# Kernel optimization log

Hardware: AMD Instinct MI355X
Metric: run time of the kernel (lower is better)

The kernel has to match this reference:

```python
import jax, jax.numpy as jnp
import numpy as np

B, T, C = 4, 2048, 1024
H = 16
D = C // H  # head_dim = 64


def setup_inputs() -> dict:
    key = jax.random.key(0)
    k1, k2, k3, k4, k5 = jax.random.split(key, 5)
    s = 1.0 / np.sqrt(C)
    return {
        "x": jax.random.normal(k1, (B, T, C), dtype=jnp.float32),
        "Wqkv": jax.random.normal(k2, (C, 3 * C), dtype=jnp.float32) * s,
        "bqkv": jax.random.normal(k3, (3 * C,), dtype=jnp.float32) * 0.02,
        "Wproj": jax.random.normal(k4, (C, C), dtype=jnp.float32) * s,
        "bproj": jax.random.normal(k5, (C,), dtype=jnp.float32) * 0.02,
    }


def reference(x, Wqkv, bqkv, Wproj, bproj):
    b, t, c = x.shape
    qkv = x @ Wqkv + bqkv                      # [B,T,3C]
    qkv = qkv.reshape(b, t, 3, H, D)
    q, k, v = (qkv[:, :, i].transpose(0, 2, 1, 3) for i in range(3))  # [B,H,T,D]
    scale = D ** -0.5
    attn = jnp.einsum("bhqd,bhkd->bhqk", q, k) * scale
    causal = jnp.tril(jnp.ones((t, t), dtype=bool))
    attn = jnp.where(causal[None, None], attn, -jnp.inf)
    attn = jax.nn.softmax(attn, axis=-1)
    out = jnp.einsum("bhqk,bhkd->bhqd", attn, v)  # [B,H,T,D]
    out = out.transpose(0, 2, 1, 3).reshape(b, t, c)
    return out @ Wproj + bproj
```

## Files before the change

kernel.cpp:

```cpp
#include <hip/hip_runtime.h>
#include <hip/hip_bf16.h>

typedef __bf16 bf16;
typedef __bf16 bf16x4 __attribute__((ext_vector_type(4)));
typedef __bf16 bf16x8 __attribute__((ext_vector_type(8)));
typedef float  f32x4  __attribute__((ext_vector_type(4)));

#define DEV static __device__ __forceinline__

static constexpr int Bsz = 4, T = 2048, C = 1024, H = 16;
static constexpr int M  = Bsz * T;
static constexpr int N1 = 3 * C;
static constexpr float SM_SCALE = 0.125f;

DEV void gload16(const bf16* g, bf16* l) {
  __builtin_amdgcn_global_load_lds(
      (const __attribute__((address_space(1))) void*)g,
      (__attribute__((address_space(3))) void*)l, 16, 0, 0);
}

__launch_bounds__(256)
__global__ void convert_kernel(const float* __restrict__ in, bf16* __restrict__ out) {
  const size_t i = ((size_t)blockIdx.x * 256 + threadIdx.x) * 8;
  f32x4 a = *(const f32x4*)(in + i);
  f32x4 b = *(const f32x4*)(in + i + 4);
  *(bf16x4*)(out + i)     = __builtin_convertvector(a, bf16x4);
  *(bf16x4*)(out + i + 4) = __builtin_convertvector(b, bf16x4);
}

__launch_bounds__(256)
__global__ void transpose_conv_kernel(const float* __restrict__ in,
                                      bf16* __restrict__ out, int K, int N) {
  __shared__ float t[32][33];
  const int n0 = blockIdx.x * 32, k0 = blockIdx.y * 32;
  const int tx = threadIdx.x & 31, ty = threadIdx.x >> 5;
#pragma unroll
  for (int j = 0; j < 4; ++j)
    t[ty + j * 8][tx] = in[(size_t)(k0 + ty + j * 8) * N + n0 + tx];
  __syncthreads();
#pragma unroll
  for (int j = 0; j < 4; ++j)
    out[(size_t)(n0 + ty + j * 8) * K + k0 + tx] = (bf16)t[tx][ty + j * 8];
}

template <bool OUT_BF16>
__launch_bounds__(256)
__global__ void gemm_kernel(const bf16* __restrict__ A,
                            const bf16* __restrict__ Bt,
                            const float* __restrict__ bias,
                            void* __restrict__ Out, int Ndim, int Kdim) {
  __shared__ bf16 lds_a[128 * 64];
  __shared__ bf16 lds_b[128 * 64];
  const int tid = threadIdx.x;
  const int l = tid & 63, wid = tid >> 6;
  const int wm = wid >> 1, wn = wid & 1;
  const int lr = l & 15, lh = l >> 4;
  const int m0 = blockIdx.x * 128, n0 = blockIdx.y * 128;
  const int r8 = l >> 3, g8 = (l & 7) * 8;

  f32x4 acc[4][4] = {};

  for (int k0 = 0; k0 < Kdim; k0 += 64) {
    __syncthreads();
#pragma unroll
    for (int i = 0; i < 4; ++i) {
      const int c = wid * 4 + i;
      const int row = c * 8 + r8;
      gload16(A  + (size_t)(m0 + row) * Kdim + k0 + g8, &lds_a[c * 512]);
      gload16(Bt + (size_t)(n0 + row) * Kdim + k0 + g8, &lds_b[c * 512]);
    }
    __syncthreads();
#pragma unroll
    for (int kk = 0; kk < 2; ++kk) {
      bf16x8 af[4], bfr[4];
#pragma unroll
      for (int mi = 0; mi < 4; ++mi)
        af[mi] = *(const bf16x8*)&lds_a[(wm * 64 + mi * 16 + lr) * 64 + kk * 32 + lh * 8];
#pragma unroll
      for (int ni = 0; ni < 4; ++ni)
        bfr[ni] = *(const bf16x8*)&lds_b[(wn * 64 + ni * 16 + lr) * 64 + kk * 32 + lh * 8];
#pragma unroll
      for (int mi = 0; mi < 4; ++mi)
#pragma unroll
        for (int ni = 0; ni < 4; ++ni)
          acc[mi][ni] = __builtin_amdgcn_mfma_f32_16x16x32_bf16(
              af[mi], bfr[ni], acc[mi][ni], 0, 0, 0);
    }
  }
#pragma unroll
  for (int ni = 0; ni < 4; ++ni) {
    int col = n0 + wn * 64 + ni * 16 + lr;
    float bv = bias[col];
#pragma unroll
    for (int mi = 0; mi < 4; ++mi) {
#pragma unroll
      for (int r = 0; r < 4; ++r) {
        int row = m0 + wm * 64 + mi * 16 + lh * 4 + r;
        float v = acc[mi][ni][r] + bv;
        if (OUT_BF16)
          ((bf16*)Out)[(size_t)row * Ndim + col] = (bf16)v;
        else
          ((float*)Out)[(size_t)row * Ndim + col] = v;
      }
    }
  }
}

DEV int vswz(int d, int key) {
  return (d * 64 + key) ^ ((((d & 7) ^ (d >> 3)) & 7) << 3);
}

__launch_bounds__(256)
__global__ void attn_kernel(const bf16* __restrict__ qkv, bf16* __restrict__ out) {
  __shared__ bf16 lds_k[2][64 * 64];
  __shared__ bf16 lds_vt[2][64 * 64];
  __shared__ bf16 lds_p[4][16 * 64];
  const int tid = threadIdx.x, l = tid & 63, w = tid >> 6;
  const int lr = l & 15, lh = l >> 4;
  const int p = blockIdx.x;
  const int bh = p >> 4, jj = p & 15;
  const int b = bh >> 4, h = bh & 15;
  const size_t RS = 3 * C;
  const bf16* base  = qkv + (size_t)b * T * RS;
  const bf16* kbase = base + C + h * 64;
  const bf16* vbase = base + 2 * C + h * 64;
  const int srow = tid >> 3;
  const int ss   = tid & 7;
  bf16* op = out + (size_t)b * T * C + h * 64;

  for (int it = 0; it < 2; ++it) {
    const int qt = it ? jj : 31 - jj;
    const int q16 = qt * 64 + w * 16;
    bf16x8 qf[2];
#pragma unroll
    for (int kk = 0; kk < 2; ++kk) {
      bf16x8 qv = *(const bf16x8*)(base + (size_t)(q16 + lr) * RS + h * 64 + kk * 32 + lh * 8);
#pragma unroll
      for (int j = 0; j < 8; ++j) qf[kk][j] = (bf16)((float)qv[j] * SM_SCALE);
    }

    float mq = -__builtin_inff(), lq = 0.f;
    f32x4 o[4] = {};

    bf16x8 pk[2], pv[2];
#pragma unroll
    for (int i = 0; i < 2; ++i) {
      int row = i * 32 + srow;
      pk[i] = *(const bf16x8*)(kbase + (size_t)row * RS + ss * 8);
      pv[i] = *(const bf16x8*)(vbase + (size_t)row * RS + ss * 8);
    }
    __syncthreads();
#pragma unroll
    for (int i = 0; i < 2; ++i) {
      int row = i * 32 + srow;
      *(bf16x8*)&lds_k[0][(row * 64 + ss * 8) ^ ((row & 7) << 3)] = pk[i];
#pragma unroll
      for (int j = 0; j < 8; ++j) lds_vt[0][vswz(ss * 8 + j, row)] = pv[i][j];
    }
    __syncthreads();

    int buf = 0;
    for (int kt = 0; kt <= qt; ++kt) {
      const bf16* kb = &lds_k[buf][0];
      const bf16* vb = &lds_vt[buf][0];
      if (kt < qt) {
#pragma unroll
        for (int i = 0; i < 2; ++i) {
          int row = i * 32 + srow;
          pk[i] = *(const bf16x8*)(kbase + (size_t)((kt + 1) * 64 + row) * RS + ss * 8);
          pv[i] = *(const bf16x8*)(vbase + (size_t)((kt + 1) * 64 + row) * RS + ss * 8);
        }
      }

      f32x4 s4[4] = {};
      __builtin_amdgcn_s_setprio(1);
#pragma unroll
      for (int kk = 0; kk < 2; ++kk) {
#pragma unroll
        for (int kn = 0; kn < 4; ++kn) {
          int key = kn * 16 + lr;
          bf16x8 kf = *(const bf16x8*)&kb[(key * 64 + kk * 32 + lh * 8) ^ ((key & 7) << 3)];
          s4[kn] = __builtin_amdgcn_mfma_f32_16x16x32_bf16(kf, qf[kk], s4[kn], 0, 0, 0);
        }
      }
      __builtin_amdgcn_s_setprio(0);
      if (kt == qt) {
        const int qloc = w * 16 + lr;
#pragma unroll
        for (int kn = 0; kn < 4; ++kn)
#pragma unroll
          for (int r = 0; r < 4; ++r)
            if ((kn * 16 + lh * 4 + r) > qloc) s4[kn][r] = -__builtin_inff();
      }
      float pm = s4[0][0];
#pragma unroll
      for (int kn = 0; kn < 4; ++kn)
#pragma unroll
        for (int r = 0; r < 4; ++r) pm = fmaxf(pm, s4[kn][r]);
      pm = fmaxf(pm, __shfl_xor(pm, 16));
      pm = fmaxf(pm, __shfl_xor(pm, 32));
      const float mnew = fmaxf(mq, pm);
      const float alpha_q = __expf(mq - mnew);
      mq = mnew;
      float ssum = 0.f;
#pragma unroll
      for (int kn = 0; kn < 4; ++kn)
#pragma unroll
        for (int r = 0; r < 4; ++r) {
          float p2 = __expf(s4[kn][r] - mnew);
          s4[kn][r] = p2;
          ssum += p2;
        }
#pragma unroll
      for (int kn = 0; kn < 4; ++kn) {
        bf16x4 pb;
#pragma unroll
        for (int r = 0; r < 4; ++r) pb[r] = (bf16)s4[kn][r];
        *(bf16x4*)&lds_p[w][(lr * 64 + kn * 16 + lh * 4) ^ ((lr & 7) << 3)] = pb;
      }
      ssum += __shfl_xor(ssum, 16);
      ssum += __shfl_xor(ssum, 32);
      lq = lq * alpha_q + ssum;
      float al[4];
#pragma unroll
      for (int r = 0; r < 4; ++r) al[r] = __shfl(alpha_q, lh * 4 + r);
#pragma unroll
      for (int ni = 0; ni < 4; ++ni)
#pragma unroll
        for (int r = 0; r < 4; ++r) o[ni][r] *= al[r];
      __builtin_amdgcn_s_setprio(1);
#pragma unroll
      for (int kk = 0; kk < 2; ++kk) {
        bf16x8 pf = *(const bf16x8*)&lds_p[w][(lr * 64 + kk * 32 + lh * 8) ^ ((lr & 7) << 3)];
#pragma unroll
        for (int ni = 0; ni < 4; ++ni) {
          int d = ni * 16 + lr;
          bf16x8 vf = *(const bf16x8*)&vb[vswz(d, kk * 32 + lh * 8)];
          o[ni] = __builtin_amdgcn_mfma_f32_16x16x32_bf16(pf, vf, o[ni], 0, 0, 0);
        }
      }
      __builtin_amdgcn_s_setprio(0);

      if (kt < qt) {
#pragma unroll
        for (int i = 0; i < 2; ++i) {
          int row = i * 32 + srow;
          *(bf16x8*)&lds_k[buf ^ 1][(row * 64 + ss * 8) ^ ((row & 7) << 3)] = pk[i];
#pragma unroll
          for (int j = 0; j < 8; ++j) lds_vt[buf ^ 1][vswz(ss * 8 + j, row)] = pv[i][j];
        }
        __syncthreads();
        buf ^= 1;
      }
    }
    float lden[4];
#pragma unroll
    for (int r = 0; r < 4; ++r) lden[r] = __shfl(lq, lh * 4 + r);
#pragma unroll
    for (int ni = 0; ni < 4; ++ni)
#pragma unroll
      for (int r = 0; r < 4; ++r) {
        int q = q16 + lh * 4 + r;
        op[(size_t)q * C + ni * 16 + lr] = (bf16)(o[ni][r] / lden[r]);
      }
  }
}

extern "C" void kernel_launch(void* const* d_in, const int* in_sizes, int n_in,
                              void* d_out, int out_size, void* d_ws, size_t ws_size,
                              hipStream_t stream) {
  const float* x     = (const float*)d_in[0];
  const float* Wqkv  = (const float*)d_in[1];
  const float* bqkv  = (const float*)d_in[2];
  const float* Wproj = (const float*)d_in[3];
  const float* bproj = (const float*)d_in[4];
  float* out = (float*)d_out;

  char* ws = (char*)d_ws;
  bf16* qkv      = (bf16*)(ws);
  bf16* wqkvt    = (bf16*)(ws + 50331648);
  bf16* wprojt   = (bf16*)(ws + 56623104);
  bf16* attn_out = (bf16*)(ws + 58720256);
  bf16* x_bf16   = attn_out;

  convert_kernel<<<dim3(M * C / (256 * 8)), 256, 0, stream>>>(x, x_bf16);
  transpose_conv_kernel<<<dim3(N1 / 32, C / 32), 256, 0, stream>>>(Wqkv, wqkvt, C, N1);
  transpose_conv_kernel<<<dim3(C / 32, C / 32), 256, 0, stream>>>(Wproj, wprojt, C, C);
  gemm_kernel<true><<<dim3(M / 128, N1 / 128), 256, 0, stream>>>(
      x_bf16, wqkvt, bqkv, qkv, N1, C);
  attn_kernel<<<dim3(Bsz * H * 16), 256, 0, stream>>>(qkv, attn_out);
  gemm_kernel<false><<<dim3(M / 128, C / 128), 256, 0, stream>>>(
      attn_out, wprojt, bproj, out, C, C);
}
```

Baseline: 300.1 us.

## Emit V pre-transposed from QKV GEMM and stream K/V via direct-to-LDS loads

The QKV GEMM epilogue now writes the V part in a per-head transposed [B,H,D,T] layout, and Q/K go to a narrower 2C-stride buffer. This lets the attention kernel fetch K and V tiles with global_load_lds straight into swizzled LDS, removing the register staging and the scalar per-element V transpose stores. The GEMM grid is also remapped so that consecutive M tiles are grouped per XCD for L2 locality. The final normalisation uses a reciprocal multiply instead of a divide. The risks are the more complex swizzle index math and uncoalesced 8-byte strided V stores in the GEMM epilogue.

```diff
diff --git a/kernel.cpp b/kernel.cpp
--- a/kernel.cpp
+++ b/kernel.cpp
@@ -13,7 +13,7 @@
 static constexpr int N1 = 3 * C;
 static constexpr float SM_SCALE = 0.125f;
 
-DEV void gload16(const bf16* g, bf16* l) {
+DEV void gload16(const bf16* g, const bf16* l) {
   __builtin_amdgcn_global_load_lds(
       (const __attribute__((address_space(1))) void*)g,
       (__attribute__((address_space(3))) void*)l, 16, 0, 0);
@@ -43,19 +43,24 @@
     out[(size_t)(n0 + ty + j * 8) * K + k0 + tx] = (bf16)t[tx][ty + j * 8];
 }
 
-template <bool OUT_BF16>
+template <bool OUT_BF16, bool V_SPLIT>
 __launch_bounds__(256)
 __global__ void gemm_kernel(const bf16* __restrict__ A,
                             const bf16* __restrict__ Bt,
                             const float* __restrict__ bias,
-                            void* __restrict__ Out, int Ndim, int Kdim) {
+                            void* __restrict__ Out, bf16* __restrict__ vt,
+                            int Ndim, int Kdim) {
   __shared__ bf16 lds_a[128 * 64];
   __shared__ bf16 lds_b[128 * 64];
   const int tid = threadIdx.x;
   const int l = tid & 63, wid = tid >> 6;
   const int wm = wid >> 1, wn = wid & 1;
   const int lr = l & 15, lh = l >> 4;
-  const int m0 = blockIdx.x * 128, n0 = blockIdx.y * 128;
+  const int gx = gridDim.x, cpx = gx >> 3;
+  const int L = blockIdx.y * gx + blockIdx.x;
+  const int xcd = L & 7, q = L >> 3;
+  const int m0 = (xcd * cpx + (q & (cpx - 1))) * 128;
+  const int n0 = (q / cpx) * 128;
   const int r8 = l >> 3, g8 = (l & 7) * 8;
 
   f32x4 acc[4][4] = {};
@@ -87,20 +92,38 @@
               af[mi], bfr[ni], acc[mi][ni], 0, 0, 0);
     }
   }
-#pragma unroll
-  for (int ni = 0; ni < 4; ++ni) {
-    int col = n0 + wn * 64 + ni * 16 + lr;
-    float bv = bias[col];
-#pragma unroll
-    for (int mi = 0; mi < 4; ++mi) {
-#pragma unroll
-      for (int r = 0; r < 4; ++r) {
-        int row = m0 + wm * 64 + mi * 16 + lh * 4 + r;
-        float v = acc[mi][ni][r] + bv;
-        if (OUT_BF16)
-          ((bf16*)Out)[(size_t)row * Ndim + col] = (bf16)v;
-        else
-          ((float*)Out)[(size_t)row * Ndim + col] = v;
+  if (V_SPLIT && n0 >= 2 * C) {
+    const int b = m0 >> 11, tb = (m0 & 2047) + wm * 64;
+#pragma unroll
+    for (int ni = 0; ni < 4; ++ni) {
+      const int col = n0 - 2 * C + wn * 64 + ni * 16 + lr;
+      const int hh = col >> 6, dd = col & 63;
+      const float bv = bias[2 * C + col];
+      bf16* vdst = vt + ((size_t)((b * H + hh) * 64 + dd)) * T + tb + lh * 4;
+#pragma unroll
+      for (int mi = 0; mi < 4; ++mi) {
+        bf16x4 p4;
+#pragma unroll
+        for (int r = 0; r < 4; ++r) p4[r] = (bf16)(acc[mi][ni][r] + bv);
+        *(bf16x4*)&vdst[mi * 16] = p4;
+      }
+    }
+  } else {
+#pragma unroll
+    for (int ni = 0; ni < 4; ++ni) {
+      const int col = n0 + wn * 64 + ni * 16 + lr;
+      const float bv = bias[col];
+#pragma unroll
+      for (int mi = 0; mi < 4; ++mi) {
+#pragma unroll
+        for (int r = 0; r < 4; ++r) {
+          const int row = m0 + wm * 64 + mi * 16 + lh * 4 + r;
+          const float v = acc[mi][ni][r] + bv;
+          if (OUT_BF16)
+            ((bf16*)Out)[(size_t)row * Ndim + col] = (bf16)v;
+          else
+            ((float*)Out)[(size_t)row * Ndim + col] = v;
+        }
       }
     }
   }
@@ -111,7 +134,9 @@
 }
 
 __launch_bounds__(256)
-__global__ void attn_kernel(const bf16* __restrict__ qkv, bf16* __restrict__ out) {
+__global__ void attn_kernel(const bf16* __restrict__ qk,
+                            const bf16* __restrict__ vt,
+                            bf16* __restrict__ out) {
   __shared__ bf16 lds_k[2][64 * 64];
   __shared__ bf16 lds_vt[2][64 * 64];
   __shared__ bf16 lds_p[4][16 * 64];
@@ -120,13 +145,13 @@
   const int p = blockIdx.x;
   const int bh = p >> 4, jj = p & 15;
   const int b = bh >> 4, h = bh & 15;
-  const size_t RS = 3 * C;
-  const bf16* base  = qkv + (size_t)b * T * RS;
+  const size_t RS = 2 * C;
+  const bf16* base  = qk + (size_t)b * T * RS;
   const bf16* kbase = base + C + h * 64;
-  const bf16* vbase = base + 2 * C + h * 64;
-  const int srow = tid >> 3;
-  const int ss   = tid & 7;
+  const bf16* vth   = vt + (size_t)bh * 64 * T;
   bf16* op = out + (size_t)b * T * C + h * 64;
+  const int r1 = tid >> 3, cc = tid & 7;
+  const int kc = cc ^ (r1 & 7);
 
   for (int it = 0; it < 2; ++it) {
     const int qt = it ? jj : 31 - jj;
@@ -142,20 +167,13 @@
     float mq = -__builtin_inff(), lq = 0.f;
     f32x4 o[4] = {};
 
-    bf16x8 pk[2], pv[2];
+    __syncthreads();
 #pragma unroll
     for (int i = 0; i < 2; ++i) {
-      int row = i * 32 + srow;
-      pk[i] = *(const bf16x8*)(kbase + (size_t)row * RS + ss * 8);
-      pv[i] = *(const bf16x8*)(vbase + (size_t)row * RS + ss * 8);
-    }
-    __syncthreads();
-#pragma unroll
-    for (int i = 0; i < 2; ++i) {
-      int row = i * 32 + srow;
-      *(bf16x8*)&lds_k[0][(row * 64 + ss * 8) ^ ((row & 7) << 3)] = pk[i];
-#pragma unroll
-      for (int j = 0; j < 8; ++j) lds_vt[0][vswz(ss * 8 + j, row)] = pv[i][j];
+      const int row = i * 32 + r1;
+      gload16(kbase + (size_t)row * RS + kc * 8, &lds_k[0][i * 2048 + w * 512]);
+      const int vc = cc ^ (((r1 & 7) ^ (i * 4 + (r1 >> 3))) & 7);
+      gload16(vth + (size_t)row * T + vc * 8, &lds_vt[0][i * 2048 + w * 512]);
     }
     __syncthreads();
 
@@ -164,11 +182,15 @@
       const bf16* kb = &lds_k[buf][0];
       const bf16* vb = &lds_vt[buf][0];
       if (kt < qt) {
+        const int nb = buf ^ 1;
 #pragma unroll
         for (int i = 0; i < 2; ++i) {
-          int row = i * 32 + srow;
-          pk[i] = *(const bf16x8*)(kbase + (size_t)((kt + 1) * 64 + row) * RS + ss * 8);
-          pv[i] = *(const bf16x8*)(vbase + (size_t)((kt + 1) * 64 + row) * RS + ss * 8);
+          const int row = i * 32 + r1;
+          gload16(kbase + (size_t)((kt + 1) * 64 + row) * RS + kc * 8,
+                  &lds_k[nb][i * 2048 + w * 512]);
+          const int vc = cc ^ (((r1 & 7) ^ (i * 4 + (r1 >> 3))) & 7);
+          gload16(vth + (size_t)row * T + (kt + 1) * 64 + vc * 8,
+                  &lds_vt[nb][i * 2048 + w * 512]);
         }
       }
 
@@ -178,7 +200,7 @@
       for (int kk = 0; kk < 2; ++kk) {
 #pragma unroll
         for (int kn = 0; kn < 4; ++kn) {
-          int key = kn * 16 + lr;
+          const int key = kn * 16 + lr;
           bf16x8 kf = *(const bf16x8*)&kb[(key * 64 + kk * 32 + lh * 8) ^ ((key & 7) << 3)];
           s4[kn] = __builtin_amdgcn_mfma_f32_16x16x32_bf16(kf, qf[kk], s4[kn], 0, 0, 0);
         }
@@ -207,7 +229,7 @@
       for (int kn = 0; kn < 4; ++kn)
 #pragma unroll
         for (int r = 0; r < 4; ++r) {
-          float p2 = __expf(s4[kn][r] - mnew);
+          const float p2 = __expf(s4[kn][r] - mnew);
           s4[kn][r] = p2;
           ssum += p2;
         }
@@ -234,7 +256,7 @@
         bf16x8 pf = *(const bf16x8*)&lds_p[w][(lr * 64 + kk * 32 + lh * 8) ^ ((lr & 7) << 3)];
 #pragma unroll
         for (int ni = 0; ni < 4; ++ni) {
-          int d = ni * 16 + lr;
+          const int d = ni * 16 + lr;
           bf16x8 vf = *(const bf16x8*)&vb[vswz(d, kk * 32 + lh * 8)];
           o[ni] = __builtin_amdgcn_mfma_f32_16x16x32_bf16(pf, vf, o[ni], 0, 0, 0);
         }
@@ -242,26 +264,19 @@
       __builtin_amdgcn_s_setprio(0);
 
       if (kt < qt) {
-#pragma unroll
-        for (int i = 0; i < 2; ++i) {
-          int row = i * 32 + srow;
-          *(bf16x8*)&lds_k[buf ^ 1][(row * 64 + ss * 8) ^ ((row & 7) << 3)] = pk[i];
-#pragma unroll
-          for (int j = 0; j < 8; ++j) lds_vt[buf ^ 1][vswz(ss * 8 + j, row)] = pv[i][j];
-        }
         __syncthreads();
         buf ^= 1;
       }
     }
-    float lden[4];
-#pragma unroll
-    for (int r = 0; r < 4; ++r) lden[r] = __shfl(lq, lh * 4 + r);
+    float lrec[4];
+#pragma unroll
+    for (int r = 0; r < 4; ++r) lrec[r] = 1.0f / __shfl(lq, lh * 4 + r);
 #pragma unroll
     for (int ni = 0; ni < 4; ++ni)
 #pragma unroll
       for (int r = 0; r < 4; ++r) {
-        int q = q16 + lh * 4 + r;
-        op[(size_t)q * C + ni * 16 + lr] = (bf16)(o[ni][r] / lden[r]);
+        const int qrow = q16 + lh * 4 + r;
+        op[(size_t)qrow * C + ni * 16 + lr] = (bf16)(o[ni][r] * lrec[r]);
       }
   }
 }
@@ -277,7 +292,8 @@
   float* out = (float*)d_out;
 
   char* ws = (char*)d_ws;
-  bf16* qkv      = (bf16*)(ws);
+  bf16* qk       = (bf16*)(ws);
+  bf16* vt       = (bf16*)(ws + 33554432);
   bf16* wqkvt    = (bf16*)(ws + 50331648);
   bf16* wprojt   = (bf16*)(ws + 56623104);
   bf16* attn_out = (bf16*)(ws + 58720256);
@@ -286,9 +302,9 @@
   convert_kernel<<<dim3(M * C / (256 * 8)), 256, 0, stream>>>(x, x_bf16);
   transpose_conv_kernel<<<dim3(N1 / 32, C / 32), 256, 0, stream>>>(Wqkv, wqkvt, C, N1);
   transpose_conv_kernel<<<dim3(C / 32, C / 32), 256, 0, stream>>>(Wproj, wprojt, C, C);
-  gemm_kernel<true><<<dim3(M / 128, N1 / 128), 256, 0, stream>>>(
-      x_bf16, wqkvt, bqkv, qkv, N1, C);
-  attn_kernel<<<dim3(Bsz * H * 16), 256, 0, stream>>>(qkv, attn_out);
-  gemm_kernel<false><<<dim3(M / 128, C / 128), 256, 0, stream>>>(
-      attn_out, wprojt, bproj, out, C, C);
-}
+  gemm_kernel<true, true><<<dim3(M / 128, N1 / 128), 256, 0, stream>>>(
+      x_bf16, wqkvt, bqkv, qk, vt, 2 * C, C);
+  attn_kernel<<<dim3(Bsz * H * 16), 256, 0, stream>>>(qk, vt, attn_out);
+  gemm_kernel<false, false><<<dim3(M / 128, C / 128), 256, 0, stream>>>(
+      attn_out, wprojt, bproj, out, nullptr, C, C);
+}
```

Result: slower. 307.7 us (+2.6%).
